# Kernel tuning notes

Hardware: AMD Instinct MI355X
Metric: run time of the kernel (lower is better)

## Reference

```python
import jax, jax.numpy as jnp
import numpy as np

B, V, C, H, W, D = 1, 3, 64, 96, 96, 48


def bilinear_sample(feat, gx, gy):
    """torch F.grid_sample(mode='bilinear', padding_mode='zeros', align_corners=True).
    feat: (B, C, H, W); gx, gy: (B, N) normalized coords in [-1, 1]. Returns (B, C, N)."""
    Bf, Cf, Hf, Wf = feat.shape
    x = (gx + 1.0) * 0.5 * (Wf - 1)
    y = (gy + 1.0) * 0.5 * (Hf - 1)
    x0 = jnp.floor(x)
    y0 = jnp.floor(y)
    wx1 = x - x0
    wy1 = y - y0
    wx0 = 1.0 - wx1
    wy0 = 1.0 - wy1
    flat = feat.reshape(Bf, Cf, Hf * Wf)

    def gather(xi, yi):
        valid = (xi >= 0) & (xi <= Wf - 1) & (yi >= 0) & (yi <= Hf - 1)
        xi_c = jnp.clip(xi, 0, Wf - 1).astype(jnp.int32)
        yi_c = jnp.clip(yi, 0, Hf - 1).astype(jnp.int32)
        idx = (yi_c * Wf + xi_c)[:, None, :]  # (B,1,N), broadcast over C
        return jnp.take_along_axis(flat, idx, axis=2) * valid[:, None, :]

    out = (gather(x0, y0) * (wx0 * wy0)[:, None]
           + gather(x0 + 1, y0) * (wx1 * wy0)[:, None]
           + gather(x0, y0 + 1) * (wx0 * wy1)[:, None]
           + gather(x0 + 1, y0 + 1) * (wx1 * wy1)[:, None])
    return out


def src_grid(proj_mat, depth_values, Hs, Ws):
    """homo_warp grid computation. proj_mat: (B,3,4); depth_values: (B,D).
    Returns normalized gx, gy each of shape (B, D*Hs*Ws)."""
    xs = jnp.arange(Ws, dtype=jnp.float32)
    ys = jnp.arange(Hs, dtype=jnp.float32)
    gx_, gy_ = jnp.meshgrid(xs, ys)  # (Hs, Ws) each
    ref = jnp.stack([gx_.ravel(), gy_.ravel(), jnp.ones(Hs * Ws, jnp.float32)], 0)  # (3, HW)
    R = proj_mat[:, :, :3]
    T = proj_mat[:, :, 3]
    # (B,3,D,HW): R @ p + T / depth
    pts = jnp.einsum('bij,jn->bin', R, ref)[:, :, None, :] + T[:, :, None, None] / depth_values[:, None, :, None]
    xy = pts[:, :2] / pts[:, 2:3]
    gx = xy[:, 0] / ((Ws - 1) / 2.0) - 1.0
    gy = xy[:, 1] / ((Hs - 1) / 2.0) - 1.0
    Bb = proj_mat.shape[0]
    return gx.reshape(Bb, -1), gy.reshape(Bb, -1)


def setup_inputs() -> dict:
    key = jax.random.key(0)
    k1, k2, k3, k4 = jax.random.split(key, 4)
    imgs = jax.random.normal(k1, (B, V, 3, H, W), jnp.float32)
    feats = jax.random.normal(k2, (B, V, C, H, W), jnp.float32)
    # near-identity projections so warped coords land mostly in-range (z ~ 1)
    eye = jnp.broadcast_to(jnp.eye(3, dtype=jnp.float32), (B, V, 3, 3))
    Rn = eye + 0.05 * jax.random.normal(k3, (B, V, 3, 3), jnp.float32)
    Tn = 0.5 * jax.random.normal(jax.random.fold_in(k3, 1), (B, V, 3, 1), jnp.float32)
    proj_mats = jnp.concatenate([Rn, Tn], axis=-1)
    depth_values = 2.0 + 4.0 * jax.random.uniform(k4, (B, D), jnp.float32)
    return {"imgs": imgs, "feats": feats, "proj_mats": proj_mats, "depth_values": depth_values}


def reference(imgs, feats, proj_mats, depth_values):
    Bb, Vv, _, Hh, Ww = imgs.shape
    Cc = feats.shape[2]
    Dd = depth_values.shape[1]
    # ref view volume (broadcast over D)
    ref_volume = jnp.broadcast_to(feats[:, 0][:, :, None], (Bb, Cc, Dd, Hh, Ww))
    volume_sum = ref_volume
    volume_sq_sum = ref_volume ** 2
    mask_sum = jnp.ones((Bb, Dd, Hh, Ww), jnp.float32)  # ref view always in-range
    img_chans = [jnp.broadcast_to(imgs[:, 0][:, :, None], (Bb, 3, Dd, Hh, Ww))]
    for i in range(Vv - 1):  # small fixed number of source views
        gx, gy = src_grid(proj_mats[:, i + 1], depth_values, Hh, Ww)
        wv = bilinear_sample(feats[:, i + 1], gx, gy).reshape(Bb, Cc, Dd, Hh, Ww)
        wi = bilinear_sample(imgs[:, i + 1], gx, gy).reshape(Bb, 3, Dd, Hh, Ww)
        m = ((gx > -1.0) & (gx < 1.0) & (gy > -1.0) & (gy < 1.0)).astype(jnp.float32).reshape(Bb, Dd, Hh, Ww)
        volume_sum = volume_sum + wv
        volume_sq_sum = volume_sq_sum + wv ** 2
        mask_sum = mask_sum + m
        img_chans.append(wi)
    count = 1.0 / mask_sum[:, None]  # (B,1,D,H,W)
    var = volume_sq_sum * count - (volume_sum * count) ** 2  # (B,C,D,H,W)
    img_chans.append(var)
    return jnp.concatenate(img_chans, axis=1)  # (B, 3*V + C, D, H, W)
```

## Files before the change

### kernel.cpp

```cpp
#include <hip/hip_runtime.h>

#define BDIM 256

constexpr int Vv = 3, Cc = 64, Hh = 96, Ww = 96, Dd = 48;
constexpr int HW = Hh * Ww;
constexpr int NPIX = Dd * HW;
constexpr int DHW = Dd * HW;
constexpr int NXCD = 8;

__device__ __forceinline__ void compute_warp(const float* __restrict__ proj, float depth,
                                             float xf, float yf,
                                             int offs[2][4], float wts[2][4], float& msum)
{
    msum = 1.0f;
#pragma unroll
    for (int v = 0; v < 2; ++v) {
#pragma clang fp contract(off)
        const float* P = proj + (v + 1) * 12;
        const float r00 = P[0], r01 = P[1], r02 = P[2],  t0 = P[3];
        const float r10 = P[4], r11 = P[5], r12 = P[6],  t1 = P[7];
        const float r20 = P[8], r21 = P[9], r22 = P[10], t2 = P[11];

        const float px = ((r00 * xf + r01 * yf) + r02) + t0 / depth;
        const float py = ((r10 * xf + r11 * yf) + r12) + t1 / depth;
        const float pz = ((r20 * xf + r21 * yf) + r22) + t2 / depth;

        const float xy0 = px / pz;
        const float xy1 = py / pz;
        const float gx = xy0 / ((float)(Ww - 1) * 0.5f) - 1.0f;
        const float gy = xy1 / ((float)(Hh - 1) * 0.5f) - 1.0f;

        const bool inb = (gx > -1.0f) && (gx < 1.0f) && (gy > -1.0f) && (gy < 1.0f);
        msum += inb ? 1.0f : 0.0f;

        const float sx = (gx + 1.0f) * 0.5f * (float)(Ww - 1);
        const float sy = (gy + 1.0f) * 0.5f * (float)(Hh - 1);
        const float x0 = floorf(sx), y0 = floorf(sy);
        const float wx1 = sx - x0, wy1 = sy - y0;
        const float wx0 = 1.0f - wx1, wy0 = 1.0f - wy1;

#pragma unroll
        for (int k = 0; k < 4; ++k) {
            const float xi = (k & 1) ? (x0 + 1.0f) : x0;
            const float yi = (k & 2) ? (y0 + 1.0f) : y0;
            const float wk = ((k & 1) ? wx1 : wx0) * ((k & 2) ? wy1 : wy0);
            const bool valid = (xi >= 0.0f) && (xi <= (float)(Ww - 1)) &&
                               (yi >= 0.0f) && (yi <= (float)(Hh - 1));
            const float xc = fminf(fmaxf(xi, 0.0f), (float)(Ww - 1));
            const float yc = fminf(fmaxf(yi, 0.0f), (float)(Hh - 1));
            offs[v][k] = (int)yc * Ww + (int)xc;
            wts[v][k] = valid ? wk : 0.0f;
        }
    }
}

__device__ __forceinline__ float var_one(float fr, float a1, float a2, float cnt)
{
    const float s  = fr + a1 + a2;
    const float q  = fr * fr + a1 * a1 + a2 * a2;
    const float sc = s * cnt;
    return q * cnt - sc * sc;
}

__global__ void __launch_bounds__(BDIM) transpose_feats_kernel(const float* __restrict__ feats,
                                                               float* __restrict__ ft)
{
    __shared__ float tile[64][65];
    const int v  = blockIdx.y;
    const int p0 = blockIdx.x * 64;
    const float* src = feats + (size_t)v * Cc * HW;

    const int px = threadIdx.x & 63;
    const int c0 = threadIdx.x >> 6;
#pragma unroll
    for (int c = c0; c < Cc; c += 4)
        tile[c][px] = src[(size_t)c * HW + p0 + px];
    __syncthreads();

    const int cc  = threadIdx.x & 63;
    const int pr0 = threadIdx.x >> 6;
    float* dst = ft + ((size_t)v * HW + p0) * Cc;
#pragma unroll
    for (int p = pr0; p < 64; p += 4)
        dst[p * Cc + cc] = tile[cc][p];
}

__global__ void __launch_bounds__(BDIM) ge_row_kernel(
    const float* __restrict__ imgs, const float* __restrict__ ftr,
    const float* __restrict__ proj, const float* __restrict__ depthv,
    float* __restrict__ out)
{
    __shared__ float s_tile[Cc][Ww + 1];
    __shared__ alignas(16) int   s_base[2][Ww][4];
    __shared__ alignas(16) float s_wt[2][Ww][4];
    __shared__ float s_cnt[Ww];

    const int nper = (Dd * Hh) / NXCD;
    const int blk  = (blockIdx.x & (NXCD - 1)) * nper + (blockIdx.x >> 3);
    const int h    = blk / Dd;
    const int d    = blk - h * Dd;
    const int tid  = threadIdx.x;
    const int rowbase = d * HW + h * Ww;

    if (tid < Ww) {
        const int w = tid;
        int offs[2][4];
        float wts[2][4];
        float msum;
        compute_warp(proj, depthv[d], (float)w, (float)h, offs, wts, msum);
        s_cnt[w] = 1.0f / msum;
#pragma unroll
        for (int v = 0; v < 2; ++v)
#pragma unroll
            for (int k = 0; k < 4; ++k) {
                s_base[v][w][k] = ((v + 1) * HW + offs[v][k]) * Cc;
                s_wt[v][w][k]   = wts[v][k];
            }

        const int hw = h * Ww + w;
#pragma unroll
        for (int c = 0; c < 3; ++c)
            out[c * DHW + rowbase + w] = imgs[c * HW + hw];

#pragma unroll
        for (int v = 0; v < 2; ++v) {
            const float* ib = imgs + (size_t)(v + 1) * 3 * HW;
#pragma unroll
            for (int c = 0; c < 3; ++c) {
                const float* p = ib + (size_t)c * HW;
                const float acc = wts[v][0] * p[offs[v][0]] + wts[v][1] * p[offs[v][1]] +
                                  wts[v][2] * p[offs[v][2]] + wts[v][3] * p[offs[v][3]];
                out[(3 * (v + 1) + c) * DHW + rowbase + w] = acc;
            }
        }
    }
    __syncthreads();

    {
        const int wave = tid >> 6;
        const int lane = tid & 63;
        const int sub  = lane >> 4;
        const int c4   = (lane & 15) << 2;
        const int p0   = wave * (Ww / 4);
#pragma unroll 2
        for (int i = 0; i < Ww / 16; ++i) {
            const int p = p0 + i * 4 + sub;
            const float cnt = s_cnt[p];
            const int4   b0 = *reinterpret_cast<const int4*>(&s_base[0][p][0]);
            const int4   b1 = *reinterpret_cast<const int4*>(&s_base[1][p][0]);
            const float4 w0 = *reinterpret_cast<const float4*>(&s_wt[0][p][0]);
            const float4 w1 = *reinterpret_cast<const float4*>(&s_wt[1][p][0]);

            const float4 fr  = *reinterpret_cast<const float4*>(ftr + (size_t)(h * Ww + p) * Cc + c4);
            const float4 v00 = *reinterpret_cast<const float4*>(ftr + b0.x + c4);
            const float4 v01 = *reinterpret_cast<const float4*>(ftr + b0.y + c4);
            const float4 v02 = *reinterpret_cast<const float4*>(ftr + b0.z + c4);
            const float4 v03 = *reinterpret_cast<const float4*>(ftr + b0.w + c4);
            const float4 v10 = *reinterpret_cast<const float4*>(ftr + b1.x + c4);
            const float4 v11 = *reinterpret_cast<const float4*>(ftr + b1.y + c4);
            const float4 v12 = *reinterpret_cast<const float4*>(ftr + b1.z + c4);
            const float4 v13 = *reinterpret_cast<const float4*>(ftr + b1.w + c4);

            {
                const float a1 = w0.x * v00.x + w0.y * v01.x + w0.z * v02.x + w0.w * v03.x;
                const float a2 = w1.x * v10.x + w1.y * v11.x + w1.z * v12.x + w1.w * v13.x;
                s_tile[c4 + 0][p] = var_one(fr.x, a1, a2, cnt);
            }
            {
                const float a1 = w0.x * v00.y + w0.y * v01.y + w0.z * v02.y + w0.w * v03.y;
                const float a2 = w1.x * v10.y + w1.y * v11.y + w1.z * v12.y + w1.w * v13.y;
                s_tile[c4 + 1][p] = var_one(fr.y, a1, a2, cnt);
            }
            {
                const float a1 = w0.x * v00.z + w0.y * v01.z + w0.z * v02.z + w0.w * v03.z;
                const float a2 = w1.x * v10.z + w1.y * v11.z + w1.z * v12.z + w1.w * v13.z;
                s_tile[c4 + 2][p] = var_one(fr.z, a1, a2, cnt);
            }
            {
                const float a1 = w0.x * v00.w + w0.y * v01.w + w0.z * v02.w + w0.w * v03.w;
                const float a2 = w1.x * v10.w + w1.y * v11.w + w1.z * v12.w + w1.w * v13.w;
                s_tile[c4 + 3][p] = var_one(fr.w, a1, a2, cnt);
            }
        }
    }
    __syncthreads();

#pragma unroll
    for (int idx = tid; idx < Cc * Ww; idx += BDIM) {
        const int cc = idx / Ww;
        const int p  = idx - cc * Ww;
        out[(9 + cc) * DHW + rowbase + p] = s_tile[cc][p];
    }
}

__global__ void __launch_bounds__(BDIM) ge_direct_kernel(
    const float* __restrict__ imgs, const float* __restrict__ feats,
    const float* __restrict__ proj, const float* __restrict__ depthv,
    float* __restrict__ out)
{
    const int idx = blockIdx.x * BDIM + threadIdx.x;
    if (idx >= NPIX) return;
    const int w = idx % Ww;
    const int t = idx / Ww;
    const int h = t % Hh;
    const int d = t / Hh;
    const int ohw = h * Ww + w;

    int offs[2][4];
    float wts[2][4];
    float msum;
    compute_warp(proj, depthv[d], (float)w, (float)h, offs, wts, msum);

    const int obase = d * HW + ohw;
#pragma unroll
    for (int c = 0; c < 3; ++c)
        out[c * DHW + obase] = imgs[c * HW + ohw];

#pragma unroll
    for (int v = 0; v < 2; ++v) {
        const float* ib = imgs + (size_t)(v + 1) * 3 * HW;
#pragma unroll
        for (int c = 0; c < 3; ++c) {
            const float* p = ib + (size_t)c * HW;
            const float acc = wts[v][0] * p[offs[v][0]] + wts[v][1] * p[offs[v][1]] +
                              wts[v][2] * p[offs[v][2]] + wts[v][3] * p[offs[v][3]];
            out[(3 * (v + 1) + c) * DHW + obase] = acc;
        }
    }

    const float count = 1.0f / msum;
    const float* f0 = feats;
    const float* f1 = feats + (size_t)Cc * HW;
    const float* f2 = feats + (size_t)2 * Cc * HW;
#pragma unroll 8
    for (int c = 0; c < Cc; ++c) {
        const float fr = f0[(size_t)c * HW + ohw];
        const float* p1 = f1 + (size_t)c * HW;
        const float* p2 = f2 + (size_t)c * HW;
        const float a1 = wts[0][0] * p1[offs[0][0]] + wts[0][1] * p1[offs[0][1]] +
                         wts[0][2] * p1[offs[0][2]] + wts[0][3] * p1[offs[0][3]];
        const float a2 = wts[1][0] * p2[offs[1][0]] + wts[1][1] * p2[offs[1][1]] +
                         wts[1][2] * p2[offs[1][2]] + wts[1][3] * p2[offs[1][3]];
        const float s = fr + a1 + a2;
        const float sq = fr * fr + a1 * a1 + a2 * a2;
        const float sc = s * count;
        out[(3 * Vv + c) * DHW + obase] = sq * count - sc * sc;
    }
}

extern "C" void kernel_launch(void* const* d_in, const int* in_sizes, int n_in,
                              void* d_out, int out_size, void* d_ws, size_t ws_size,
                              hipStream_t stream)
{
    const float* imgs   = (const float*)d_in[0];
    const float* feats  = (const float*)d_in[1];
    const float* proj   = (const float*)d_in[2];
    const float* depthv = (const float*)d_in[3];
    float* out = (float*)d_out;

    const size_t need = (size_t)Vv * HW * Cc * sizeof(float);

    if (ws_size >= need) {
        float* ftr = (float*)d_ws;
        dim3 g1(HW / 64, Vv);
        transpose_feats_kernel<<<g1, BDIM, 0, stream>>>(feats, ftr);
        ge_row_kernel<<<Dd * Hh, BDIM, 0, stream>>>(imgs, ftr, proj, depthv, out);
    } else {
        const int blocks = (NPIX + BDIM - 1) / BDIM;
        ge_direct_kernel<<<blocks, BDIM, 0, stream>>>(imgs, feats, proj, depthv, out);
    }
}
```

Measured before the change: 182.9 us.

## Write variance directly to global and split warp computation per view

```diff
diff --git a/kernel.cpp b/kernel.cpp
--- a/kernel.cpp
+++ b/kernel.cpp
@@ -8,6 +8,47 @@
 constexpr int DHW = Dd * HW;
 constexpr int NXCD = 8;
 
+__device__ __forceinline__ void compute_warp_v(const float* __restrict__ P, float depth,
+                                               float xf, float yf,
+                                               int offs[4], float wts[4], float& inbf)
+{
+#pragma clang fp contract(off)
+    const float r00 = P[0], r01 = P[1], r02 = P[2],  t0 = P[3];
+    const float r10 = P[4], r11 = P[5], r12 = P[6],  t1 = P[7];
+    const float r20 = P[8], r21 = P[9], r22 = P[10], t2 = P[11];
+
+    const float px = ((r00 * xf + r01 * yf) + r02) + t0 / depth;
+    const float py = ((r10 * xf + r11 * yf) + r12) + t1 / depth;
+    const float pz = ((r20 * xf + r21 * yf) + r22) + t2 / depth;
+
+    const float xy0 = px / pz;
+    const float xy1 = py / pz;
+    const float gx = xy0 / ((float)(Ww - 1) * 0.5f) - 1.0f;
+    const float gy = xy1 / ((float)(Hh - 1) * 0.5f) - 1.0f;
+
+    const bool inb = (gx > -1.0f) && (gx < 1.0f) && (gy > -1.0f) && (gy < 1.0f);
+    inbf = inb ? 1.0f : 0.0f;
+
+    const float sx = (gx + 1.0f) * 0.5f * (float)(Ww - 1);
+    const float sy = (gy + 1.0f) * 0.5f * (float)(Hh - 1);
+    const float x0 = floorf(sx), y0 = floorf(sy);
+    const float wx1 = sx - x0, wy1 = sy - y0;
+    const float wx0 = 1.0f - wx1, wy0 = 1.0f - wy1;
+
+#pragma unroll
+    for (int k = 0; k < 4; ++k) {
+        const float xi = (k & 1) ? (x0 + 1.0f) : x0;
+        const float yi = (k & 2) ? (y0 + 1.0f) : y0;
+        const float wk = ((k & 1) ? wx1 : wx0) * ((k & 2) ? wy1 : wy0);
+        const bool valid = (xi >= 0.0f) && (xi <= (float)(Ww - 1)) &&
+                           (yi >= 0.0f) && (yi <= (float)(Hh - 1));
+        const float xc = fminf(fmaxf(xi, 0.0f), (float)(Ww - 1));
+        const float yc = fminf(fmaxf(yi, 0.0f), (float)(Hh - 1));
+        offs[k] = (int)yc * Ww + (int)xc;
+        wts[k] = valid ? wk : 0.0f;
+    }
+}
+
 __device__ __forceinline__ void compute_warp(const float* __restrict__ proj, float depth,
                                              float xf, float yf,
                                              int offs[2][4], float wts[2][4], float& msum)
@@ -15,42 +56,9 @@
     msum = 1.0f;
 #pragma unroll
     for (int v = 0; v < 2; ++v) {
-#pragma clang fp contract(off)
-        const float* P = proj + (v + 1) * 12;
-        const float r00 = P[0], r01 = P[1], r02 = P[2],  t0 = P[3];
-        const float r10 = P[4], r11 = P[5], r12 = P[6],  t1 = P[7];
-        const float r20 = P[8], r21 = P[9], r22 = P[10], t2 = P[11];
-
-        const float px = ((r00 * xf + r01 * yf) + r02) + t0 / depth;
-        const float py = ((r10 * xf + r11 * yf) + r12) + t1 / depth;
-        const float pz = ((r20 * xf + r21 * yf) + r22) + t2 / depth;
-
-        const float xy0 = px / pz;
-        const float xy1 = py / pz;
-        const float gx = xy0 / ((float)(Ww - 1) * 0.5f) - 1.0f;
-        const float gy = xy1 / ((float)(Hh - 1) * 0.5f) - 1.0f;
-
-        const bool inb = (gx > -1.0f) && (gx < 1.0f) && (gy > -1.0f) && (gy < 1.0f);
-        msum += inb ? 1.0f : 0.0f;
-
-        const float sx = (gx + 1.0f) * 0.5f * (float)(Ww - 1);
-        const float sy = (gy + 1.0f) * 0.5f * (float)(Hh - 1);
-        const float x0 = floorf(sx), y0 = floorf(sy);
-        const float wx1 = sx - x0, wy1 = sy - y0;
-        const float wx0 = 1.0f - wx1, wy0 = 1.0f - wy1;
-
-#pragma unroll
-        for (int k = 0; k < 4; ++k) {
-            const float xi = (k & 1) ? (x0 + 1.0f) : x0;
-            const float yi = (k & 2) ? (y0 + 1.0f) : y0;
-            const float wk = ((k & 1) ? wx1 : wx0) * ((k & 2) ? wy1 : wy0);
-            const bool valid = (xi >= 0.0f) && (xi <= (float)(Ww - 1)) &&
-                               (yi >= 0.0f) && (yi <= (float)(Hh - 1));
-            const float xc = fminf(fmaxf(xi, 0.0f), (float)(Ww - 1));
-            const float yc = fminf(fmaxf(yi, 0.0f), (float)(Hh - 1));
-            offs[v][k] = (int)yc * Ww + (int)xc;
-            wts[v][k] = valid ? wk : 0.0f;
-        }
+        float inb;
+        compute_warp_v(proj + (v + 1) * 12, depth, xf, yf, offs[v], wts[v], inb);
+        msum += inb;
     }
 }
 
@@ -90,10 +98,9 @@
     const float* __restrict__ proj, const float* __restrict__ depthv,
     float* __restrict__ out)
 {
-    __shared__ float s_tile[Cc][Ww + 1];
     __shared__ alignas(16) int   s_base[2][Ww][4];
     __shared__ alignas(16) float s_wt[2][Ww][4];
-    __shared__ float s_cnt[Ww];
+    __shared__ float s_inb[2][Ww];
 
     const int nper = (Dd * Hh) / NXCD;
     const int blk  = (blockIdx.x & (NXCD - 1)) * nper + (blockIdx.x >> 3);
@@ -102,37 +109,34 @@
     const int tid  = threadIdx.x;
     const int rowbase = d * HW + h * Ww;
 
+    if (tid < 2 * Ww) {
+        const int v = (tid >= Ww) ? 1 : 0;
+        const int w = tid - v * Ww;
+        int offs[4];
+        float wts[4];
+        float inb;
+        compute_warp_v(proj + (v + 1) * 12, depthv[d], (float)w, (float)h, offs, wts, inb);
+        s_inb[v][w] = inb;
+#pragma unroll
+        for (int k = 0; k < 4; ++k) {
+            s_base[v][w][k] = ((v + 1) * HW + offs[k]) * Cc;
+            s_wt[v][w][k]   = wts[k];
+        }
+
+        const float* ib = imgs + (size_t)(v + 1) * 3 * HW;
+#pragma unroll
+        for (int c = 0; c < 3; ++c) {
+            const float* p = ib + (size_t)c * HW;
+            const float acc = wts[0] * p[offs[0]] + wts[1] * p[offs[1]] +
+                              wts[2] * p[offs[2]] + wts[3] * p[offs[3]];
+            out[(3 * (v + 1) + c) * DHW + rowbase + w] = acc;
+        }
+    }
     if (tid < Ww) {
-        const int w = tid;
-        int offs[2][4];
-        float wts[2][4];
-        float msum;
-        compute_warp(proj, depthv[d], (float)w, (float)h, offs, wts, msum);
-        s_cnt[w] = 1.0f / msum;
-#pragma unroll
-        for (int v = 0; v < 2; ++v)
-#pragma unroll
-            for (int k = 0; k < 4; ++k) {
-                s_base[v][w][k] = ((v + 1) * HW + offs[v][k]) * Cc;
-                s_wt[v][w][k]   = wts[v][k];
-            }
-
-        const int hw = h * Ww + w;
+        const int hw = h * Ww + tid;
 #pragma unroll
         for (int c = 0; c < 3; ++c)
-            out[c * DHW + rowbase + w] = imgs[c * HW + hw];
-
-#pragma unroll
-        for (int v = 0; v < 2; ++v) {
-            const float* ib = imgs + (size_t)(v + 1) * 3 * HW;
-#pragma unroll
-            for (int c = 0; c < 3; ++c) {
-                const float* p = ib + (size_t)c * HW;
-                const float acc = wts[v][0] * p[offs[v][0]] + wts[v][1] * p[offs[v][1]] +
-                                  wts[v][2] * p[offs[v][2]] + wts[v][3] * p[offs[v][3]];
-                out[(3 * (v + 1) + c) * DHW + rowbase + w] = acc;
-            }
-        }
+            out[c * DHW + rowbase + tid] = imgs[c * HW + hw];
     }
     __syncthreads();
 
@@ -142,10 +146,11 @@
         const int sub  = lane >> 4;
         const int c4   = (lane & 15) << 2;
         const int p0   = wave * (Ww / 4);
+        float* outv = out + (size_t)9 * DHW + rowbase;
 #pragma unroll 2
         for (int i = 0; i < Ww / 16; ++i) {
             const int p = p0 + i * 4 + sub;
-            const float cnt = s_cnt[p];
+            const float cnt = 1.0f / (1.0f + s_inb[0][p] + s_inb[1][p]);
             const int4   b0 = *reinterpret_cast<const int4*>(&s_base[0][p][0]);
             const int4   b1 = *reinterpret_cast<const int4*>(&s_base[1][p][0]);
             const float4 w0 = *reinterpret_cast<const float4*>(&s_wt[0][p][0]);
@@ -164,32 +169,24 @@
             {
                 const float a1 = w0.x * v00.x + w0.y * v01.x + w0.z * v02.x + w0.w * v03.x;
                 const float a2 = w1.x * v10.x + w1.y * v11.x + w1.z * v12.x + w1.w * v13.x;
-                s_tile[c4 + 0][p] = var_one(fr.x, a1, a2, cnt);
+                outv[(size_t)(c4 + 0) * DHW + p] = var_one(fr.x, a1, a2, cnt);
             }
             {
                 const float a1 = w0.x * v00.y + w0.y * v01.y + w0.z * v02.y + w0.w * v03.y;
                 const float a2 = w1.x * v10.y + w1.y * v11.y + w1.z * v12.y + w1.w * v13.y;
-                s_tile[c4 + 1][p] = var_one(fr.y, a1, a2, cnt);
+                outv[(size_t)(c4 + 1) * DHW + p] = var_one(fr.y, a1, a2, cnt);
             }
             {
                 const float a1 = w0.x * v00.z + w0.y * v01.z + w0.z * v02.z + w0.w * v03.z;
                 const float a2 = w1.x * v10.z + w1.y * v11.z + w1.z * v12.z + w1.w * v13.z;
-                s_tile[c4 + 2][p] = var_one(fr.z, a1, a2, cnt);
+                outv[(size_t)(c4 + 2) * DHW + p] = var_one(fr.z, a1, a2, cnt);
             }
             {
                 const float a1 = w0.x * v00.w + w0.y * v01.w + w0.z * v02.w + w0.w * v03.w;
                 const float a2 = w1.x * v10.w + w1.y * v11.w + w1.z * v12.w + w1.w * v13.w;
-                s_tile[c4 + 3][p] = var_one(fr.w, a1, a2, cnt);
-            }
-        }
-    }
-    __syncthreads();
-
-#pragma unroll
-    for (int idx = tid; idx < Cc * Ww; idx += BDIM) {
-        const int cc = idx / Ww;
-        const int p  = idx - cc * Ww;
-        out[(9 + cc) * DHW + rowbase + p] = s_tile[cc][p];
+                outv[(size_t)(c4 + 3) * DHW + p] = var_one(fr.w, a1, a2, cnt);
+            }
+        }
     }
 }
 
```

After: 225.0 us. +23.0%, slower.
